# Kernel tuning notes

Measured on AMD Instinct MI355X. Metric: run time of the kernel, lower is better.

Reference implementation:

```python
import jax, jax.numpy as jnp
import numpy as np

LN_EPS = 1e-5
WKV_EPS = 1e-8
NEG_INF = -1e38


def _layernorm(x, g, b):
    m = jnp.mean(x, axis=-1, keepdims=True)
    v = jnp.mean(jnp.square(x - m), axis=-1, keepdims=True)
    return (x - m) * jax.lax.rsqrt(v + LN_EPS) * g + b


def _wkv(w, u, k, v):
    """RWKV WKV linear recurrence with log-sum-exp stabilized state.
    w,u: (C,); k,v: (B,T,C). Returns y (B,T,C), new_state (B,C,2)."""
    B, T, C = k.shape
    aa0 = jnp.zeros((B, C), k.dtype)
    bb0 = jnp.full((B, C), NEG_INF, k.dtype)

    def step(carry, kv_t):
        aa, bb = carry
        kk, vv = kv_t  # (B,C) each
        ww = u + kk
        p = jnp.maximum(bb, ww)
        e1 = jnp.exp(bb - p)
        e2 = jnp.exp(ww - p)
        y_t = (e1 * aa + e2 * vv) / (e1 + e2 + WKV_EPS)
        ww = w + bb
        p = jnp.maximum(ww, kk)
        e1 = jnp.exp(ww - p)
        e2 = jnp.exp(kk - p)
        aa = e1 * aa + e2 * vv
        bb = p + jnp.log(e1 + e2 + WKV_EPS)
        return (aa, bb), y_t

    (aa, bb), ys = jax.lax.scan(step, (aa0, bb0),
                                (jnp.swapaxes(k, 0, 1), jnp.swapaxes(v, 0, 1)))
    y = jnp.swapaxes(ys, 0, 1)  # (B,T,C)
    new_state = jnp.stack([aa, bb], axis=-1)  # (B,C,2)
    return y, new_state


def setup_inputs() -> dict:
    key = jax.random.key(0)
    ks = jax.random.split(key, 12)
    B, T, C = 8, 2048, 1024
    scale = 0.02
    return {
        "x": jax.random.normal(ks[0], (B, T, C), jnp.float32),
        "time_decay": jax.random.uniform(ks[1], (C,), jnp.float32, -1.0, 1.0),
        "time_first": jax.random.uniform(ks[2], (C,), jnp.float32, -1.0, 1.0),
        "W_tm": jax.random.normal(ks[3], (C, 3 * C), jnp.float32) * scale,
        "g1": jnp.ones((C,), jnp.float32),
        "b1": jnp.zeros((C,), jnp.float32),
        "tmk": jax.random.uniform(ks[4], (1, 1, C), jnp.float32),
        "tmv": jax.random.uniform(ks[5], (1, 1, C), jnp.float32),
        "tmr": jax.random.uniform(ks[6], (1, 1, C), jnp.float32),
        "W_cm": jax.random.normal(ks[7], (C, 4 * C), jnp.float32) * scale,
        "W_cp": jax.random.normal(ks[8], (4 * C, C), jnp.float32) * scale,
        "g2": jnp.ones((C,), jnp.float32),
        "b2": jnp.zeros((C,), jnp.float32),
        "cmk": jax.random.uniform(ks[9], (1, 1, C), jnp.float32),
        "cmr": jax.random.uniform(ks[10], (1, 1, C), jnp.float32),
    }


def reference(x, time_decay, time_first, W_tm, g1, b1, tmk, tmv, tmr,
              W_cm, W_cp, g2, b2, cmk, cmr):
    # ---- time mixing ----
    x_prev = jnp.concatenate([x[:, :1], x[:, :-1]], axis=1)  # shift (state=None)
    kvr = _layernorm(x, g1, b1) @ W_tm  # (B,T,3C)
    k, v, r = jnp.split(kvr, 3, axis=-1)
    k = k * tmk + x_prev * (1.0 - tmk)
    v = v * tmv + x_prev * (1.0 - tmv)
    r = jax.nn.sigmoid(r * tmr + x_prev * (1.0 - tmr))
    y, new_state = _wkv(time_decay, time_first, k, v)
    x = x + r * y
    # ---- channel mixing ----
    xp = jnp.concatenate([x[:, -1:], x[:, :-1]], axis=1)  # as in source
    xn = _layernorm(x, g2, b2)
    kk = xn @ W_cm  # (B,T,4C) hidden
    cmk4 = jnp.tile(cmk, (1, 1, 4))
    xp4 = jnp.tile(xp, (1, 1, 4))
    kk = kk * cmk4 + xp4 * (1.0 - cmk4)
    rr = jax.nn.sigmoid(xn * cmr + xp * (1.0 - cmr))
    vv = jnp.square(jax.nn.relu(kk)) @ W_cp  # (B,T,C)
    x = x + rr * vv
    return x, new_state
```

## Files before the change

### kernel.cpp

```cpp
#include <hip/hip_runtime.h>


#define Bb 8
#define T 2048
#define C 1024
#define M (Bb*T)
#define LCH 32
#define NCH 64
#define NCI (Bb*NCH)
#define WKV_THREADS (NCI*C)

typedef unsigned short u16;
typedef unsigned int u32;
typedef __bf16 bf16x8 __attribute__((ext_vector_type(8)));
typedef float f32x4 __attribute__((ext_vector_type(4)));
typedef u16 u16x4 __attribute__((ext_vector_type(4)));

__device__ __forceinline__ u16 f2bf(float f) {
    u32 u = __float_as_uint(f);
    u32 r = u + 0x7FFFu + ((u >> 16) & 1u);
    return (u16)(r >> 16);
}
__device__ __forceinline__ float bf2f(u16 s) {
    return __uint_as_float(((u32)s) << 16);
}
__device__ __forceinline__ float sigmoidf_(float z) {
    return 1.0f / (1.0f + __expf(-z));
}
__device__ __forceinline__ void load_lds16(const void* g, void* l) {
    __builtin_amdgcn_global_load_lds(
        (const __attribute__((address_space(1))) void*)g,
        (__attribute__((address_space(3))) void*)l, 16, 0, 0);
}

__global__ __launch_bounds__(256) void transpose_cast_kernel(
    const float* __restrict__ W, u16* __restrict__ Wt, int K, int N)
{
    __shared__ float tile[32][33];
    const int bk = blockIdx.x * 32, bn = blockIdx.y * 32;
    const int tx = threadIdx.x, ty = threadIdx.y;
    #pragma unroll
    for (int i = 0; i < 32; i += 8)
        tile[ty + i][tx] = W[(size_t)(bk + ty + i) * N + bn + tx];
    __syncthreads();
    #pragma unroll
    for (int i = 0; i < 32; i += 8)
        Wt[(size_t)(bn + ty + i) * K + bk + tx] = f2bf(tile[tx][ty + i]);
}

__device__ __forceinline__ void gemm256_mainloop(
    const u16* __restrict__ A, const int lda,
    const u16* __restrict__ Bt, const int ldb, const int nkt,
    const int m0, const int n0, u16* lds, f32x4 acc[2][2][4][2])
{
    const int tid  = threadIdx.x;
    const int wave = tid >> 6, lane = tid & 63;
    const int q = lane >> 4, m16 = lane & 15;
    const int wm = wave >> 2, wn = wave & 3;

    const f32x4 zero4 = {0.f, 0.f, 0.f, 0.f};
    #pragma unroll
    for (int i = 0; i < 2; ++i)
        #pragma unroll
        for (int j = 0; j < 2; ++j)
            #pragma unroll
            for (int k = 0; k < 4; ++k)
                #pragma unroll
                for (int l = 0; l < 2; ++l) acc[i][j][k][l] = zero4;

    const int sr = tid >> 3;
    const int kc = ((tid & 7) ^ (sr & 7)) << 3;
    const size_t abase = (size_t)(m0 + sr) * lda + kc;
    const size_t bbase = (size_t)(n0 + sr) * ldb + kc;
    const size_t lda64 = (size_t)lda << 6, ldb64 = (size_t)ldb << 6;
    char* ldsb = (char*)lds;
    const int dst0 = tid << 4;

#define STG_A(bufs, hf, k0) do { \
    char* d_ = ldsb + (((bufs) * 4 + (hf)) << 14) + dst0; \
    const u16* g_ = A + abase + (size_t)(hf) * 2 * lda64 + (k0); \
    load_lds16(g_, d_); load_lds16(g_ + lda64, d_ + 8192); } while (0)
#define STG_B(bufs, hf, k0) do { \
    char* d_ = ldsb + (((bufs) * 4 + 2 + (hf)) << 14) + dst0; \
    const u16* g_ = Bt + bbase + (size_t)(hf) * 2 * ldb64 + (k0); \
    load_lds16(g_, d_); load_lds16(g_ + ldb64, d_ + 8192); } while (0)

    STG_A(0, 0, 0);  STG_B(0, 0, 0);  STG_A(0, 1, 0);  STG_B(0, 1, 0);
    STG_A(1, 0, 64); STG_B(1, 0, 64);
    asm volatile("s_waitcnt vmcnt(4)" ::: "memory");
    __builtin_amdgcn_s_barrier();

    const int arow = ((wm << 6) + m16) << 6;
    const int brow = ((wn << 5) + m16) << 6;
    const int xh = m16 & 7;
    const int ch0 = (q ^ xh) << 3, ch1 = ((4 + q) ^ xh) << 3;

    #pragma unroll 1
    for (int kt2 = 0; kt2 < nkt; kt2 += 2) {
        #pragma unroll
        for (int p = 0; p < 8; ++p) {
            const int pp = p & 3, aa = pp >> 1, bbq = pp & 1, buf = p >> 2;
            const u16* Ap = lds + ((buf * 4 + aa) << 13) + arow;
            const u16* Bq = lds + ((buf * 4 + 2 + bbq) << 13) + brow;
            bf16x8 av[4][2], bv[2][2];
            #pragma unroll
            for (int mf = 0; mf < 4; ++mf) {
                av[mf][0] = *(const bf16x8*)&Ap[mf * 1024 + ch0];
                av[mf][1] = *(const bf16x8*)&Ap[mf * 1024 + ch1];
            }
            #pragma unroll
            for (int nf = 0; nf < 2; ++nf) {
                bv[nf][0] = *(const bf16x8*)&Bq[nf * 1024 + ch0];
                bv[nf][1] = *(const bf16x8*)&Bq[nf * 1024 + ch1];
            }
            {
                const int k1 = ((kt2 + 1) & (nkt - 1)) << 6;
                const int k2 = ((kt2 + 2) & (nkt - 1)) << 6;
                const int k3 = ((kt2 + 3) & (nkt - 1)) << 6;
                if (p == 0)      STG_A(1, 1, k1);
                else if (p == 1) STG_B(1, 1, k1);
                else if (p == 2) STG_A(0, 0, k2);
                else if (p == 3) STG_B(0, 0, k2);
                else if (p == 4) STG_A(0, 1, k2);
                else if (p == 5) STG_B(0, 1, k2);
                else if (p == 6) STG_A(1, 0, k3);
                else             STG_B(1, 0, k3);
            }
            __builtin_amdgcn_s_barrier();
            asm volatile("s_waitcnt lgkmcnt(0)" ::: "memory");
            __builtin_amdgcn_s_setprio(1);
            #pragma unroll
            for (int mf = 0; mf < 4; ++mf)
                #pragma unroll
                for (int nf = 0; nf < 2; ++nf) {
                    acc[aa][bbq][mf][nf] = __builtin_amdgcn_mfma_f32_16x16x32_bf16(
                        av[mf][0], bv[nf][0], acc[aa][bbq][mf][nf], 0, 0, 0);
                    acc[aa][bbq][mf][nf] = __builtin_amdgcn_mfma_f32_16x16x32_bf16(
                        av[mf][1], bv[nf][1], acc[aa][bbq][mf][nf], 0, 0, 0);
                }
            __builtin_amdgcn_s_setprio(0);
            if (pp == 3) asm volatile("s_waitcnt vmcnt(4)" ::: "memory");
            __builtin_amdgcn_s_barrier();
        }
    }
    asm volatile("s_waitcnt vmcnt(0)" ::: "memory");
#undef STG_A
#undef STG_B
}

__global__ __launch_bounds__(256) void ln1_kernel(
    const float* __restrict__ x, const float* __restrict__ g, const float* __restrict__ b,
    u16* __restrict__ xn)
{
    const int row = blockIdx.x, tid = threadIdx.x;
    const size_t base = (size_t)row * C;
    const int c = tid * 4;
    float4 v = *(const float4*)&x[base + c];
    float s  = v.x + v.y + v.z + v.w;
    float s2 = v.x*v.x + v.y*v.y + v.z*v.z + v.w*v.w;
    #pragma unroll
    for (int off = 32; off >= 1; off >>= 1) { s += __shfl_xor(s, off); s2 += __shfl_xor(s2, off); }
    __shared__ float red[8];
    const int wave = tid >> 6, lane = tid & 63;
    if (lane == 0) { red[wave] = s; red[4 + wave] = s2; }
    __syncthreads();
    const float sum  = red[0] + red[1] + red[2] + red[3];
    const float sums = red[4] + red[5] + red[6] + red[7];
    const float mean = sum * (1.0f / C);
    const float var  = sums * (1.0f / C) - mean * mean;
    const float rstd = rsqrtf(var + 1e-5f);
    float4 gv = *(const float4*)&g[c];
    float4 bv = *(const float4*)&b[c];
    u16x4 o;
    o.x = f2bf((v.x - mean) * rstd * gv.x + bv.x);
    o.y = f2bf((v.y - mean) * rstd * gv.y + bv.y);
    o.z = f2bf((v.z - mean) * rstd * gv.z + bv.z);
    o.w = f2bf((v.w - mean) * rstd * gv.w + bv.w);
    *(u16x4*)&xn[base + c] = o;
}

__global__ __launch_bounds__(512, 2) void gemm1_kernel(
    const u16* __restrict__ xn, const u16* __restrict__ wt,
    const float* __restrict__ x,
    const float* __restrict__ tmk, const float* __restrict__ tmv, const float* __restrict__ tmr,
    u16* __restrict__ kvbuf, u16* __restrict__ rbuf)
{
    __shared__ __align__(16) u16 lds[8 * 8192];
    f32x4 acc[2][2][4][2];
    const int nbn = 12;
    int id = blockIdx.x;
    id = (id & 7) * (768 >> 3) + (id >> 3);
    const int m0 = (id / nbn) << 8, n0 = (id % nbn) << 8;
    gemm256_mainloop(xn, C, wt, C, 16, m0, n0, lds, acc);

    const int tid = threadIdx.x, wave = tid >> 6, lane = tid & 63;
    const int q = lane >> 4, m16 = lane & 15;
    const int wm = wave >> 2, wn = wave & 3;
    const int grp = n0 >> 10;
    #pragma unroll
    for (int a2 = 0; a2 < 2; ++a2)
    #pragma unroll
    for (int mf = 0; mf < 4; ++mf)
    #pragma unroll
    for (int rg = 0; rg < 4; ++rg) {
        const int row = m0 + a2 * 128 + wm * 64 + mf * 16 + q * 4 + rg;
        const int t = row & (T - 1);
        const size_t rowp = (size_t)(t ? row - 1 : row) * C;
        #pragma unroll
        for (int b2 = 0; b2 < 2; ++b2)
        #pragma unroll
        for (int nf = 0; nf < 2; ++nf) {
            const int cc = (n0 + b2 * 128 + wn * 32 + nf * 16 + m16) & (C - 1);
            const float val = acc[a2][b2][mf][nf][rg];
            const float xp = x[rowp + cc];
            if (grp == 0) {
                const float f = tmk[cc];
                kvbuf[(size_t)row * 2048 + 2 * cc] = f2bf(val * f + xp * (1.0f - f));
            } else if (grp == 1) {
                const float f = tmv[cc];
                kvbuf[(size_t)row * 2048 + 2 * cc + 1] = f2bf(val * f + xp * (1.0f - f));
            } else {
                const float f = tmr[cc];
                rbuf[(size_t)row * C + cc] = f2bf(sigmoidf_(val * f + xp * (1.0f - f)));
            }
        }
    }
}

__global__ __launch_bounds__(256) void wkv_k1(
    const u32* __restrict__ kvp, const float* __restrict__ wdec, float* __restrict__ bc)
{
    const int tid = blockIdx.x * 256 + threadIdx.x;
    const int c = tid & (C - 1), ci = tid >> 10;
    const float w = wdec[c];
    const size_t L = ((size_t)(ci >> 6) * T + (size_t)(ci & (NCH - 1)) * LCH) * C + c;
    float bb = -1e38f;
    #pragma unroll 4
    for (int t = 0; t < LCH; ++t) {
        const float k = bf2f((u16)(kvp[L + (size_t)t * C] & 0xffffu));
        const float ww = w + bb;
        const float p = fmaxf(ww, k);
        const float e1 = __expf(ww - p), e2 = __expf(k - p);
        bb = p + __logf(e1 + e2 + 1e-8f);
    }
    bc[tid] = bb;
}

__global__ __launch_bounds__(256) void wkv_p1(
    const float* __restrict__ bc, const float* __restrict__ wdec, float* __restrict__ bbin)
{
    const int gid = blockIdx.x * 256 + threadIdx.x;
    const int c = gid & (C - 1), b = gid >> 10;
    const float Lw = (float)LCH * wdec[c];
    float bb = -1e38f;
    #pragma unroll 8
    for (int j = 0; j < NCH; ++j) {
        const int idx = (b * NCH + j) * C + c;
        bbin[idx] = bb;
        const float a = Lw + bb;
        const float bcv = bc[idx];
        const float m = fmaxf(a, bcv);
        bb = m + __logf(__expf(a - m) + __expf(bcv - m));
    }
}

__global__ __launch_bounds__(256) void wkv_k2a(
    const u32* __restrict__ kvp, const float* __restrict__ wdec,
    const float* __restrict__ bbin, float* __restrict__ logS, float* __restrict__ Rr)
{
    const int tid = blockIdx.x * 256 + threadIdx.x;
    const int c = tid & (C - 1), ci = tid >> 10;
    const float w = wdec[c];
    const size_t L = ((size_t)(ci >> 6) * T + (size_t)(ci & (NCH - 1)) * LCH) * C + c;
    float bb = bbin[tid], ls = 0.0f, R = 0.0f;
    #pragma unroll 4
    for (int t = 0; t < LCH; ++t) {
        const u32 kv = kvp[L + (size_t)t * C];
        const float k = bf2f((u16)(kv & 0xffffu)), v = bf2f((u16)(kv >> 16));
        const float ww = w + bb;
        const float p = fmaxf(ww, k);
        const float e1 = __expf(ww - p), e2 = __expf(k - p);
        R = e1 * R + e2 * v;
        ls += ww - p;
        bb = p + __logf(e1 + e2 + 1e-8f);
    }
    logS[tid] = ls;
    Rr[tid] = R;
}

__global__ __launch_bounds__(256) void wkv_p2(
    const float* __restrict__ logS, const float* __restrict__ Rr, float* __restrict__ aain)
{
    const int gid = blockIdx.x * 256 + threadIdx.x;
    const int c = gid & (C - 1), b = gid >> 10;
    float a = 0.0f;
    #pragma unroll 8
    for (int j = 0; j < NCH; ++j) {
        const int idx = (b * NCH + j) * C + c;
        aain[idx] = a;
        a = __expf(logS[idx]) * a + Rr[idx];
    }
}

__global__ __launch_bounds__(256) void wkv_k2c(
    const u32* __restrict__ kvp, const u16* __restrict__ rbuf, const float* __restrict__ x,
    const float* __restrict__ wdec, const float* __restrict__ ufirst,
    const float* __restrict__ bbin, const float* __restrict__ aain,
    float* __restrict__ x2, float* __restrict__ state)
{
    const int tid = blockIdx.x * 256 + threadIdx.x;
    const int c = tid & (C - 1), ci = tid >> 10;
    const int b = ci >> 6, j = ci & (NCH - 1);
    const float w = wdec[c], u = ufirst[c];
    float aa = aain[tid], bb = bbin[tid];
    const size_t L = ((size_t)b * T + (size_t)j * LCH) * C + c;
    #pragma unroll 4
    for (int t = 0; t < LCH; ++t) {
        const size_t idx = L + (size_t)t * C;
        const u32 kv = kvp[idx];
        const float k = bf2f((u16)(kv & 0xffffu)), v = bf2f((u16)(kv >> 16));
        const float r = bf2f(rbuf[idx]), xv = x[idx];
        float ww = u + k;
        float p  = fmaxf(bb, ww);
        float e1 = __expf(bb - p), e2 = __expf(ww - p);
        const float y = (e1 * aa + e2 * v) / (e1 + e2 + 1e-8f);
        x2[idx] = xv + r * y;
        ww = w + bb;
        p  = fmaxf(ww, k);
        e1 = __expf(ww - p); e2 = __expf(k - p);
        aa = e1 * aa + e2 * v;
        bb = p + __logf(e1 + e2 + 1e-8f);
    }
    if (j == NCH - 1) {
        state[2 * (b * C + c)]     = aa;
        state[2 * (b * C + c) + 1] = bb;
    }
}

__global__ __launch_bounds__(256) void ln2_kernel(
    const float* __restrict__ x2, const float* __restrict__ g, const float* __restrict__ b,
    const float* __restrict__ cmr, u16* __restrict__ xn, u16* __restrict__ rr,
    u16* __restrict__ xps)
{
    const int row = blockIdx.x, tid = threadIdx.x;
    const size_t base = (size_t)row * C;
    const int t = row & (T - 1);
    const size_t basep = (size_t)(row - t + (t ? t - 1 : T - 1)) * C;
    const int c = tid * 4;
    float4 v = *(const float4*)&x2[base + c];
    float s  = v.x + v.y + v.z + v.w;
    float s2 = v.x*v.x + v.y*v.y + v.z*v.z + v.w*v.w;
    #pragma unroll
    for (int off = 32; off >= 1; off >>= 1) { s += __shfl_xor(s, off); s2 += __shfl_xor(s2, off); }
    __shared__ float red[8];
    const int wave = tid >> 6, lane = tid & 63;
    if (lane == 0) { red[wave] = s; red[4 + wave] = s2; }
    __syncthreads();
    const float sum  = red[0] + red[1] + red[2] + red[3];
    const float sums = red[4] + red[5] + red[6] + red[7];
    const float mean = sum * (1.0f / C);
    const float var  = sums * (1.0f / C) - mean * mean;
    const float rstd = rsqrtf(var + 1e-5f);
    float4 gv = *(const float4*)&g[c];
    float4 bv = *(const float4*)&b[c];
    float4 fv = *(const float4*)&cmr[c];
    float4 xp = *(const float4*)&x2[basep + c];
    float xn0 = (v.x - mean) * rstd * gv.x + bv.x;
    float xn1 = (v.y - mean) * rstd * gv.y + bv.y;
    float xn2 = (v.z - mean) * rstd * gv.z + bv.z;
    float xn3 = (v.w - mean) * rstd * gv.w + bv.w;
    u16x4 o; o.x = f2bf(xn0); o.y = f2bf(xn1); o.z = f2bf(xn2); o.w = f2bf(xn3);
    *(u16x4*)&xn[base + c] = o;
    u16x4 p4; p4.x = f2bf(xp.x); p4.y = f2bf(xp.y); p4.z = f2bf(xp.z); p4.w = f2bf(xp.w);
    *(u16x4*)&xps[base + c] = p4;
    u16x4 r4;
    r4.x = f2bf(sigmoidf_(xn0 * fv.x + xp.x * (1.0f - fv.x)));
    r4.y = f2bf(sigmoidf_(xn1 * fv.y + xp.y * (1.0f - fv.y)));
    r4.z = f2bf(sigmoidf_(xn2 * fv.z + xp.z * (1.0f - fv.z)));
    r4.w = f2bf(sigmoidf_(xn3 * fv.w + xp.w * (1.0f - fv.w)));
    *(u16x4*)&rr[base + c] = r4;
}

__global__ __launch_bounds__(512, 2) void gemm2_kernel(
    const u16* __restrict__ xn, const u16* __restrict__ wt,
    const u16* __restrict__ xps, const float* __restrict__ cmk,
    u16* __restrict__ hbuf, const int nbase)
{
    __shared__ __align__(16) u16 lds[8 * 8192];
    f32x4 acc[2][2][4][2];
    const int nbn = 8;
    int id = blockIdx.x;
    id = (id & 7) * (512 >> 3) + (id >> 3);
    const int m0 = (id / nbn) << 8, n0 = (id % nbn) << 8;
    gemm256_mainloop(xn, C, wt, C, 16, m0, n0, lds, acc);

    const int tid = threadIdx.x, wave = tid >> 6, lane = tid & 63;
    const int q = lane >> 4, m16 = lane & 15;
    const int wm = wave >> 2, wn = wave & 3;
    #pragma unroll
    for (int a2 = 0; a2 < 2; ++a2)
    #pragma unroll
    for (int mf = 0; mf < 4; ++mf)
    #pragma unroll
    for (int rg = 0; rg < 4; ++rg) {
        const int row = m0 + a2 * 128 + wm * 64 + mf * 16 + q * 4 + rg;
        #pragma unroll
        for (int b2 = 0; b2 < 2; ++b2)
        #pragma unroll
        for (int nf = 0; nf < 2; ++nf) {
            const int nloc = n0 + b2 * 128 + wn * 32 + nf * 16 + m16;
            const int cc = (nbase + nloc) & (C - 1);
            const float f = cmk[cc];
            const float xp = bf2f(xps[(size_t)row * C + cc]);
            const float kk = acc[a2][b2][mf][nf][rg] * f + xp * (1.0f - f);
            const float h = fmaxf(kk, 0.0f);
            hbuf[(size_t)row * 2048 + nloc] = f2bf(h * h);
        }
    }
}

__global__ __launch_bounds__(512, 2) void gemm3_kernel(
    const u16* __restrict__ hbuf, const u16* __restrict__ wt,
    const u16* __restrict__ rr, float* __restrict__ out)
{
    __shared__ __align__(16) u16 lds[8 * 8192];
    f32x4 acc[2][2][4][2];
    const int nbn = 4;
    int id = blockIdx.x;
    id = (id & 7) * (256 >> 3) + (id >> 3);
    const int m0 = (id / nbn) << 8, n0 = (id % nbn) << 8;
    gemm256_mainloop(hbuf, 2048, wt, 4096, 32, m0, n0, lds, acc);

    const int tid = threadIdx.x, wave = tid >> 6, lane = tid & 63;
    const int q = lane >> 4, m16 = lane & 15;
    const int wm = wave >> 2, wn = wave & 3;
    #pragma unroll
    for (int a2 = 0; a2 < 2; ++a2)
    #pragma unroll
    for (int mf = 0; mf < 4; ++mf)
    #pragma unroll
    for (int rg = 0; rg < 4; ++rg) {
        const int row = m0 + a2 * 128 + wm * 64 + mf * 16 + q * 4 + rg;
        #pragma unroll
        for (int b2 = 0; b2 < 2; ++b2)
        #pragma unroll
        for (int nf = 0; nf < 2; ++nf) {
            const int cc = n0 + b2 * 128 + wn * 32 + nf * 16 + m16;
            const size_t idx = (size_t)row * C + cc;
            const float base = out[idx];
            out[idx] = base + bf2f(rr[idx]) * acc[a2][b2][mf][nf][rg];
        }
    }
}

#define OFF_WT_CM  0
#define OFF_WT_CP  8388608
#define OFF_XN     16777216
#define OFF_KV     50331648
#define OFF_H      OFF_KV
#define OFF_RB     117440512
#define OFF_WT_TM  150994944
#define OFF_BC     150994944
#define OFF_BBIN   153092096
#define OFF_LOGS   155189248
#define OFF_RCH    157286400
#define OFF_AAIN   159383552
#define OFF_XPS    150994944

extern "C" void kernel_launch(void* const* d_in, const int* in_sizes, int n_in,
                              void* d_out, int out_size, void* d_ws, size_t ws_size,
                              hipStream_t stream) {
    const float* x          = (const float*)d_in[0];
    const float* time_decay = (const float*)d_in[1];
    const float* time_first = (const float*)d_in[2];
    const float* W_tm       = (const float*)d_in[3];
    const float* g1         = (const float*)d_in[4];
    const float* b1         = (const float*)d_in[5];
    const float* tmk        = (const float*)d_in[6];
    const float* tmv        = (const float*)d_in[7];
    const float* tmr        = (const float*)d_in[8];
    const float* W_cm       = (const float*)d_in[9];
    const float* W_cp       = (const float*)d_in[10];
    const float* g2         = (const float*)d_in[11];
    const float* b2         = (const float*)d_in[12];
    const float* cmk        = (const float*)d_in[13];
    const float* cmr        = (const float*)d_in[14];
    float* out = (float*)d_out;

    char* ws = (char*)d_ws;
    u16*   wt_cm = (u16*)(ws + OFF_WT_CM);
    u16*   wt_cp = (u16*)(ws + OFF_WT_CP);
    u16*   xn    = (u16*)(ws + OFF_XN);
    u16*   kvbuf = (u16*)(ws + OFF_KV);
    u16*   hbuf  = (u16*)(ws + OFF_H);
    u16*   rbuf  = (u16*)(ws + OFF_RB);
    u16*   wt_tm = (u16*)(ws + OFF_WT_TM);
    u16*   xps   = (u16*)(ws + OFF_XPS);
    float* bc    = (float*)(ws + OFF_BC);
    float* bbin  = (float*)(ws + OFF_BBIN);
    float* logS  = (float*)(ws + OFF_LOGS);
    float* Rch   = (float*)(ws + OFF_RCH);
    float* aain  = (float*)(ws + OFF_AAIN);
    float* x2    = out;

    transpose_cast_kernel<<<dim3(1024/32, 3072/32), dim3(32, 8), 0, stream>>>(W_tm, wt_tm, 1024, 3072);
    transpose_cast_kernel<<<dim3(1024/32, 4096/32), dim3(32, 8), 0, stream>>>(W_cm, wt_cm, 1024, 4096);
    transpose_cast_kernel<<<dim3(4096/32, 1024/32), dim3(32, 8), 0, stream>>>(W_cp, wt_cp, 4096, 1024);
    ln1_kernel<<<M, 256, 0, stream>>>(x, g1, b1, xn);
    gemm1_kernel<<<768, 512, 0, stream>>>(xn, wt_tm, x, tmk, tmv, tmr, kvbuf, rbuf);
    {
        const u32* kvp = (const u32*)kvbuf;
        wkv_k1 <<<WKV_THREADS/256, 256, 0, stream>>>(kvp, time_decay, bc);
        wkv_p1 <<<(Bb*C)/256, 256, 0, stream>>>(bc, time_decay, bbin);
        wkv_k2a<<<WKV_THREADS/256, 256, 0, stream>>>(kvp, time_decay, bbin, logS, Rch);
        wkv_p2 <<<(Bb*C)/256, 256, 0, stream>>>(logS, Rch, aain);
        wkv_k2c<<<WKV_THREADS/256, 256, 0, stream>>>(kvp, rbuf, x, time_decay, time_first,
                                                     bbin, aain, x2, out + (size_t)M * C);
    }
    ln2_kernel<<<M, 256, 0, stream>>>(x2, g2, b2, cmr, xn, rbuf, xps);
    for (int half = 0; half < 2; ++half) {
        const int nbase = half * 2048;
        gemm2_kernel<<<512, 512, 0, stream>>>(
            xn, wt_cm + (size_t)nbase * C, xps, cmk, hbuf, nbase);
        gemm3_kernel<<<256, 512, 0, stream>>>(
            hbuf, wt_cp + nbase, rbuf, out);
    }
}
```

Measured before the change: 862.9 us.

## Remap GEMM warp tiles so each wave reuses A/B fragments across phases

Reassigns each wave to a contiguous 128-row by 64-column subtile inside one A half and one B half. Fragments are loaded from LDS only in phases 0 and 1 and reused across the four MFMA phases, roughly halving LDS read traffic. The global-to-LDS staging order and the vmcnt/lgkmcnt waits are reshuffled to match, and all three GEMM epilogues are remapped to the new accumulator layout. Keeping double fragment buffers raises register pressure, and the partial lgkmcnt wait adds ordering risk.

```diff
diff --git a/kernel.cpp b/kernel.cpp
--- a/kernel.cpp
+++ b/kernel.cpp
@@ -86,60 +86,76 @@
     load_lds16(g_, d_); load_lds16(g_ + ldb64, d_ + 8192); } while (0)
 
     STG_A(0, 0, 0);  STG_B(0, 0, 0);  STG_A(0, 1, 0);  STG_B(0, 1, 0);
-    STG_A(1, 0, 64); STG_B(1, 0, 64);
-    asm volatile("s_waitcnt vmcnt(4)" ::: "memory");
+    STG_A(1, 0, 64);
+    asm volatile("s_waitcnt vmcnt(2)" ::: "memory");
     __builtin_amdgcn_s_barrier();
 
-    const int arow = ((wm << 6) + m16) << 6;
-    const int brow = ((wn << 5) + m16) << 6;
     const int xh = m16 & 7;
-    const int ch0 = (q ^ xh) << 3, ch1 = ((4 + q) ^ xh) << 3;
+    const int ch0 = ((q ^ xh) << 3), ch1 = (((4 + q) ^ xh) << 3);
+    const int bcol = (wn & 1) << 6;
 
     #pragma unroll 1
     for (int kt2 = 0; kt2 < nkt; kt2 += 2) {
+        bf16x8 av[2][4][2], bv[2][2][2];
         #pragma unroll
         for (int p = 0; p < 8; ++p) {
-            const int pp = p & 3, aa = pp >> 1, bbq = pp & 1, buf = p >> 2;
-            const u16* Ap = lds + ((buf * 4 + aa) << 13) + arow;
-            const u16* Bq = lds + ((buf * 4 + 2 + bbq) << 13) + brow;
-            bf16x8 av[4][2], bv[2][2];
-            #pragma unroll
-            for (int mf = 0; mf < 4; ++mf) {
-                av[mf][0] = *(const bf16x8*)&Ap[mf * 1024 + ch0];
-                av[mf][1] = *(const bf16x8*)&Ap[mf * 1024 + ch1];
-            }
-            #pragma unroll
-            for (int nf = 0; nf < 2; ++nf) {
-                bv[nf][0] = *(const bf16x8*)&Bq[nf * 1024 + ch0];
-                bv[nf][1] = *(const bf16x8*)&Bq[nf * 1024 + ch1];
+            const int buf = p >> 2, ph = p & 3;
+            const u16* Asl = lds + ((buf * 4 + wm) << 13);
+            const u16* Bsl = lds + ((buf * 4 + 2 + (wn >> 1)) << 13);
+            if (ph == 0) {
+                #pragma unroll
+                for (int mf = 0; mf < 4; ++mf) {
+                    av[0][mf][0] = *(const bf16x8*)&Asl[(mf * 16 + m16) * 64 + ch0];
+                    av[0][mf][1] = *(const bf16x8*)&Asl[(mf * 16 + m16) * 64 + ch1];
+                }
+                #pragma unroll
+                for (int nf = 0; nf < 2; ++nf) {
+                    bv[0][nf][0] = *(const bf16x8*)&Bsl[(bcol + nf * 16 + m16) * 64 + ch0];
+                    bv[0][nf][1] = *(const bf16x8*)&Bsl[(bcol + nf * 16 + m16) * 64 + ch1];
+                }
+            } else if (ph == 1) {
+                #pragma unroll
+                for (int mf = 0; mf < 4; ++mf) {
+                    av[1][mf][0] = *(const bf16x8*)&Asl[(64 + mf * 16 + m16) * 64 + ch0];
+                    av[1][mf][1] = *(const bf16x8*)&Asl[(64 + mf * 16 + m16) * 64 + ch1];
+                }
+                #pragma unroll
+                for (int nf = 0; nf < 2; ++nf) {
+                    bv[1][nf][0] = *(const bf16x8*)&Bsl[(bcol + 32 + nf * 16 + m16) * 64 + ch0];
+                    bv[1][nf][1] = *(const bf16x8*)&Bsl[(bcol + 32 + nf * 16 + m16) * 64 + ch1];
+                }
             }
             {
                 const int k1 = ((kt2 + 1) & (nkt - 1)) << 6;
                 const int k2 = ((kt2 + 2) & (nkt - 1)) << 6;
                 const int k3 = ((kt2 + 3) & (nkt - 1)) << 6;
-                if (p == 0)      STG_A(1, 1, k1);
-                else if (p == 1) STG_B(1, 1, k1);
-                else if (p == 2) STG_A(0, 0, k2);
-                else if (p == 3) STG_B(0, 0, k2);
-                else if (p == 4) STG_A(0, 1, k2);
-                else if (p == 5) STG_B(0, 1, k2);
-                else if (p == 6) STG_A(1, 0, k3);
-                else             STG_B(1, 0, k3);
+                if (p == 0)      STG_B(1, 0, k1);
+                else if (p == 1) STG_A(1, 1, k1);
+                else if (p == 2) STG_B(1, 1, k1);
+                else if (p == 3) STG_A(0, 0, k2);
+                else if (p == 4) STG_B(0, 0, k2);
+                else if (p == 5) STG_A(0, 1, k2);
+                else if (p == 6) STG_B(0, 1, k2);
+                else             STG_A(1, 0, k3);
             }
             __builtin_amdgcn_s_barrier();
-            asm volatile("s_waitcnt lgkmcnt(0)" ::: "memory");
+            if (ph == 1) asm volatile("s_waitcnt lgkmcnt(4)" ::: "memory");
+            else         asm volatile("s_waitcnt lgkmcnt(0)" ::: "memory");
             __builtin_amdgcn_s_setprio(1);
-            #pragma unroll
-            for (int mf = 0; mf < 4; ++mf)
+            {
+                const int a = ph & 1, s = ph >> 1;
                 #pragma unroll
-                for (int nf = 0; nf < 2; ++nf) {
-                    acc[aa][bbq][mf][nf] = __builtin_amdgcn_mfma_f32_16x16x32_bf16(
-                        av[mf][0], bv[nf][0], acc[aa][bbq][mf][nf], 0, 0, 0);
-                    acc[aa][bbq][mf][nf] = __builtin_amdgcn_mfma_f32_16x16x32_bf16(
-                        av[mf][1], bv[nf][1], acc[aa][bbq][mf][nf], 0, 0, 0);
-                }
+                for (int mf = 0; mf < 4; ++mf)
+                    #pragma unroll
+                    for (int nf = 0; nf < 2; ++nf) {
+                        acc[a][s][mf][nf] = __builtin_amdgcn_mfma_f32_16x16x32_bf16(
+                            av[a][mf][0], bv[s][nf][0], acc[a][s][mf][nf], 0, 0, 0);
+                        acc[a][s][mf][nf] = __builtin_amdgcn_mfma_f32_16x16x32_bf16(
+                            av[a][mf][1], bv[s][nf][1], acc[a][s][mf][nf], 0, 0, 0);
+                    }
+            }
             __builtin_amdgcn_s_setprio(0);
-            if (pp == 3) asm volatile("s_waitcnt vmcnt(4)" ::: "memory");
+            if (ph == 3) asm volatile("s_waitcnt vmcnt(2)" ::: "memory");
             __builtin_amdgcn_s_barrier();
         }
     }
@@ -198,20 +214,20 @@
     const int wm = wave >> 2, wn = wave & 3;
     const int grp = n0 >> 10;
     #pragma unroll
-    for (int a2 = 0; a2 < 2; ++a2)
+    for (int a = 0; a < 2; ++a)
     #pragma unroll
     for (int mf = 0; mf < 4; ++mf)
     #pragma unroll
     for (int rg = 0; rg < 4; ++rg) {
-        const int row = m0 + a2 * 128 + wm * 64 + mf * 16 + q * 4 + rg;
+        const int row = m0 + wm * 128 + a * 64 + mf * 16 + q * 4 + rg;
         const int t = row & (T - 1);
         const size_t rowp = (size_t)(t ? row - 1 : row) * C;
         #pragma unroll
-        for (int b2 = 0; b2 < 2; ++b2)
+        for (int s = 0; s < 2; ++s)
         #pragma unroll
         for (int nf = 0; nf < 2; ++nf) {
-            const int cc = (n0 + b2 * 128 + wn * 32 + nf * 16 + m16) & (C - 1);
-            const float val = acc[a2][b2][mf][nf][rg];
+            const int cc = (n0 + wn * 64 + s * 32 + nf * 16 + m16) & (C - 1);
+            const float val = acc[a][s][mf][nf][rg];
             const float xp = x[rowp + cc];
             if (grp == 0) {
                 const float f = tmk[cc];
@@ -398,21 +414,21 @@
     const int q = lane >> 4, m16 = lane & 15;
     const int wm = wave >> 2, wn = wave & 3;
     #pragma unroll
-    for (int a2 = 0; a2 < 2; ++a2)
+    for (int a = 0; a < 2; ++a)
     #pragma unroll
     for (int mf = 0; mf < 4; ++mf)
     #pragma unroll
     for (int rg = 0; rg < 4; ++rg) {
-        const int row = m0 + a2 * 128 + wm * 64 + mf * 16 + q * 4 + rg;
-        #pragma unroll
-        for (int b2 = 0; b2 < 2; ++b2)
+        const int row = m0 + wm * 128 + a * 64 + mf * 16 + q * 4 + rg;
+        #pragma unroll
+        for (int s = 0; s < 2; ++s)
         #pragma unroll
         for (int nf = 0; nf < 2; ++nf) {
-            const int nloc = n0 + b2 * 128 + wn * 32 + nf * 16 + m16;
+            const int nloc = n0 + wn * 64 + s * 32 + nf * 16 + m16;
             const int cc = (nbase + nloc) & (C - 1);
             const float f = cmk[cc];
             const float xp = bf2f(xps[(size_t)row * C + cc]);
-            const float kk = acc[a2][b2][mf][nf][rg] * f + xp * (1.0f - f);
+            const float kk = acc[a][s][mf][nf][rg] * f + xp * (1.0f - f);
             const float h = fmaxf(kk, 0.0f);
             hbuf[(size_t)row * 2048 + nloc] = f2bf(h * h);
         }
@@ -435,20 +451,20 @@
     const int q = lane >> 4, m16 = lane & 15;
     const int wm = wave >> 2, wn = wave & 3;
     #pragma unroll
-    for (int a2 = 0; a2 < 2; ++a2)
+    for (int a = 0; a < 2; ++a)
     #pragma unroll
     for (int mf = 0; mf < 4; ++mf)
     #pragma unroll
     for (int rg = 0; rg < 4; ++rg) {
-        const int row = m0 + a2 * 128 + wm * 64 + mf * 16 + q * 4 + rg;
-        #pragma unroll
-        for (int b2 = 0; b2 < 2; ++b2)
+        const int row = m0 + wm * 128 + a * 64 + mf * 16 + q * 4 + rg;
+        #pragma unroll
+        for (int s = 0; s < 2; ++s)
         #pragma unroll
         for (int nf = 0; nf < 2; ++nf) {
-            const int cc = n0 + b2 * 128 + wn * 32 + nf * 16 + m16;
+            const int cc = n0 + wn * 64 + s * 32 + nf * 16 + m16;
             const size_t idx = (size_t)row * C + cc;
             const float base = out[idx];
-            out[idx] = base + bf2f(rr[idx]) * acc[a2][b2][mf][nf][rg];
+            out[idx] = base + bf2f(rr[idx]) * acc[a][s][mf][nf][rg];
         }
     }
 }
```

Result: slower. 1.615 ms (+87.2%).
